# Kernel tuning notes

Measured on AMD Instinct MI355X. Metric: run time of the kernel, lower is better.

The kernel has to match this reference:

```python
import jax, jax.numpy as jnp
import numpy as np

B, S, D = 16, 2048, 128

def setup_inputs() -> dict:
    key = jax.random.key(0)
    kq, kk, kv = jax.random.split(key, 3)
    return {
        "query": jax.random.normal(kq, (B, S, D), dtype=jnp.float32),
        "key": jax.random.normal(kk, (B, S, D), dtype=jnp.float32),
        "value": jax.random.normal(kv, (B, S, D), dtype=jnp.float32),
    }

def reference(query, key, value):
    # query: (B, S2, d), key: (B, S1, d), value: (B, S1, d)
    d_k = query.shape[-1]
    scale = 1.0 / jnp.sqrt(jnp.asarray(d_k, dtype=query.dtype))
    # (B, S2, S1) attention scores
    att = jnp.einsum('bqd,bkd->bqk', query, key) * scale
    att = jax.nn.softmax(att, axis=-1)
    # (B, S2, d_v)
    return jnp.einsum('bqk,bkd->bqd', att, value)
```

## Files before the change

kernel.cpp:

```cpp
#include <hip/hip_runtime.h>

#define B_N 16
#define S_LEN 2048
#define D_DIM 128
#define TK 32
#define NTH 32

typedef __attribute__((ext_vector_type(16))) float f32x16;
typedef __attribute__((ext_vector_type(8)))  short short8;
typedef __attribute__((ext_vector_type(4)))  int   i32x4;
typedef const __attribute__((address_space(1))) void* gp1;
typedef __attribute__((address_space(3))) void* sp3;
#define GLL(g, l) __builtin_amdgcn_global_load_lds((gp1)(const void*)(g), (sp3)(void*)(l), 16, 0, 0)

static __device__ __forceinline__ unsigned short f2bf(float f) {
  unsigned u = __builtin_bit_cast(unsigned, f);
  return (unsigned short)((u + 0x7fffu + ((u >> 16) & 1u)) >> 16);
}

__global__ __launch_bounds__(256)
void prep_kernel(const float* __restrict__ K, const float* __restrict__ V,
                 unsigned short* __restrict__ Kb, unsigned short* __restrict__ VT) {
  __shared__ unsigned short lds[64 * 66];
  int bx = blockIdx.x;
  int t  = threadIdx.x;
  if (bx < 1024) {
#pragma unroll
    for (int rep = 0; rep < 4; ++rep) {
      size_t i = (((size_t)rep * 1024 + bx) * 256 + t) * 4;
      float4 v = *(const float4*)(K + i);
      unsigned lo = (unsigned)f2bf(v.x) | ((unsigned)f2bf(v.y) << 16);
      unsigned hi = (unsigned)f2bf(v.z) | ((unsigned)f2bf(v.w) << 16);
      *(uint2*)(Kb + i) = make_uint2(lo, hi);
    }
  } else {
    int bi = bx - 1024;
    int b  = bi & 15;
    int st = (bi >> 4) & 31;
    int dt = bi >> 9;
    const float* Vb = V + ((size_t)b * S_LEN + st * 64) * D_DIM + dt * 64;
    unsigned short* VTb = VT + ((size_t)b * D_DIM + dt * 64) * S_LEN + st * 64;
#pragma unroll
    for (int rep = 0; rep < 4; ++rep) {
      int idx = rep * 256 + t;
      int i  = idx >> 4;
      int j4 = (idx & 15) * 4;
      float4 v = *(const float4*)(Vb + (size_t)i * D_DIM + j4);
      unsigned lo = (unsigned)f2bf(v.x) | ((unsigned)f2bf(v.y) << 16);
      unsigned hi = (unsigned)f2bf(v.z) | ((unsigned)f2bf(v.w) << 16);
      *(uint2*)&lds[i * 66 + j4] = make_uint2(lo, hi);
    }
    __syncthreads();
#pragma unroll
    for (int rep = 0; rep < 4; ++rep) {
      int idx = rep * 256 + t;
      int dd = idx >> 4;
      int s4 = (idx & 15) * 4;
      unsigned short e0 = lds[(s4 + 0) * 66 + dd];
      unsigned short e1 = lds[(s4 + 1) * 66 + dd];
      unsigned short e2 = lds[(s4 + 2) * 66 + dd];
      unsigned short e3 = lds[(s4 + 3) * 66 + dd];
      *(uint2*)(VTb + (size_t)dd * S_LEN + s4) =
          make_uint2((unsigned)e0 | ((unsigned)e1 << 16),
                     (unsigned)e2 | ((unsigned)e3 << 16));
    }
  }
}

__global__ __launch_bounds__(512, 2)
void attn_kernel(const float* __restrict__ Q, const unsigned short* __restrict__ Kb,
                 const unsigned short* __restrict__ VT, float* __restrict__ O) {
  __shared__ __align__(16) char smem[131072];

  const int tid  = threadIdx.x;
  const int wave = tid >> 6;
  const int g    = wave >> 2;
  const int w4   = wave & 3;
  const int lane = tid & 63;
  const int l32  = lane & 31;
  const int half = lane >> 5;

  const int i     = blockIdx.x;
  const int b     = (i & 7) * 2 + ((i >> 3) & 1);
  const int qtile = i >> 4;
  const int qbase = qtile * 128 + w4 * 32;

  const float* Qb = Q + (size_t)b * S_LEN * D_DIM;
  const unsigned short* Kbb = Kb + (size_t)b * S_LEN * D_DIM;
  const unsigned short* VTb = VT + (size_t)b * D_DIM * S_LEN;

  unsigned short* kb0 = (unsigned short*)smem + (size_t)g * 4 * 4096;
  unsigned short* vb0 = (unsigned short*)(smem + 65536) + (size_t)g * 4 * 4096;

#define ISSUE_TILE(tt, buf)                                                        \
  {                                                                                \
    const int T_ = g * NTH + (tt);                                                 \
    _Pragma("unroll")                                                              \
    for (int cc = 0; cc < 2; ++cc) {                                               \
      int c = w4 * 2 + cc;                                                         \
      int rl = 4 * c + (lane >> 4);                                                \
      int lbk = (lane & 15) ^ (rl & 15);                                           \
      GLL(Kbb + (size_t)(T_ * TK + rl) * D_DIM + lbk * 8, kb0 + (buf) * 4096 + c * 512); \
      int dv = 16 * c + (lane >> 2);                                               \
      int lbv = (lane & 3) ^ ((dv >> 1) & 3);                                      \
      GLL(VTb + (size_t)dv * S_LEN + T_ * TK + lbv * 8, vb0 + (buf) * 4096 + c * 512);   \
    }                                                                              \
  }

#define QK_TILE(buf, saccv)                                                        \
  {                                                                                \
    const unsigned short* kbc_ = kb0 + (buf) * 4096;                               \
    __builtin_amdgcn_s_setprio(1);                                                 \
    _Pragma("unroll")                                                              \
    for (int ks = 0; ks < 8; ++ks) {                                               \
      int pk = (ks * 2 + half) ^ (l32 & 15);                                       \
      short8 kf = *(const short8*)&kbc_[l32 * D_DIM + pk * 8];                     \
      saccv = __builtin_amdgcn_mfma_f32_32x32x16_bf16(kf, qa[ks], saccv, 0, 0, 0); \
    }                                                                              \
    __builtin_amdgcn_s_setprio(0);                                                 \
  }

#define SOFTMAX(saccv, pf0v, pf1v)                                                 \
  {                                                                                \
    float p_[16];                                                                  \
    _Pragma("unroll")                                                              \
    for (int reg = 0; reg < 16; ++reg) {                                           \
      p_[reg] = exp2f(saccv[reg] * SC);                                            \
      lsum += p_[reg];                                                             \
    }                                                                              \
    int dw_[8];                                                                    \
    _Pragma("unroll")                                                              \
    for (int i2 = 0; i2 < 8; ++i2)                                                 \
      asm("v_cvt_pk_bf16_f32 %0, %1, %2"                                           \
          : "=v"(dw_[i2]) : "v"(p_[2 * i2]), "v"(p_[2 * i2 + 1]));                 \
    asm("v_permlane32_swap_b32 %0, %1" : "+v"(dw_[0]), "+v"(dw_[2]));              \
    asm("v_permlane32_swap_b32 %0, %1" : "+v"(dw_[1]), "+v"(dw_[3]));              \
    asm("v_permlane32_swap_b32 %0, %1" : "+v"(dw_[4]), "+v"(dw_[6]));              \
    asm("v_permlane32_swap_b32 %0, %1" : "+v"(dw_[5]), "+v"(dw_[7]));              \
    i32x4 f0_ = {dw_[0], dw_[1], dw_[2], dw_[3]};                                  \
    i32x4 f1_ = {dw_[4], dw_[5], dw_[6], dw_[7]};                                  \
    pf0v = __builtin_bit_cast(short8, f0_);                                        \
    pf1v = __builtin_bit_cast(short8, f1_);                                        \
  }

#define PV_TILE(buf, pf0v, pf1v)                                                   \
  {                                                                                \
    const unsigned short* vbc_ = vb0 + (buf) * 4096;                               \
    __builtin_amdgcn_s_setprio(1);                                                 \
    _Pragma("unroll")                                                              \
    for (int dt = 0; dt < 4; ++dt) {                                               \
      int dv = dt * 32 + l32;                                                      \
      int pv0 = half ^ ((dv >> 1) & 3);                                            \
      short8 vf0 = *(const short8*)&vbc_[dv * TK + pv0 * 8];                       \
      oacc[dt] = __builtin_amdgcn_mfma_f32_32x32x16_bf16(pf0v, vf0, oacc[dt], 0, 0, 0); \
      int pv1 = (2 + half) ^ ((dv >> 1) & 3);                                      \
      short8 vf1 = *(const short8*)&vbc_[dv * TK + pv1 * 8];                       \
      oacc[dt] = __builtin_amdgcn_mfma_f32_32x32x16_bf16(pf1v, vf1, oacc[dt], 0, 0, 0); \
    }                                                                              \
    __builtin_amdgcn_s_setprio(0);                                                 \
  }

  short8 qa[8];
  {
    const float* qp = Qb + (size_t)(qbase + l32) * D_DIM + half * 8;
#pragma unroll
    for (int ks = 0; ks < 8; ++ks) {
      float4 a0 = *(const float4*)(qp + ks * 16);
      float4 a1 = *(const float4*)(qp + ks * 16 + 4);
      short8 f;
      f[0] = (short)f2bf(a0.x); f[1] = (short)f2bf(a0.y);
      f[2] = (short)f2bf(a0.z); f[3] = (short)f2bf(a0.w);
      f[4] = (short)f2bf(a1.x); f[5] = (short)f2bf(a1.y);
      f[6] = (short)f2bf(a1.z); f[7] = (short)f2bf(a1.w);
      qa[ks] = f;
    }
  }

  ISSUE_TILE(0, 0)
  ISSUE_TILE(1, 1)
  ISSUE_TILE(2, 2)

  const f32x16 zf16 = {0.f,0.f,0.f,0.f,0.f,0.f,0.f,0.f,0.f,0.f,0.f,0.f,0.f,0.f,0.f,0.f};
  f32x16 oacc[4];
  float lsum = 0.f;
#pragma unroll
  for (int dt = 0; dt < 4; ++dt) oacc[dt] = zf16;

  const float SC = 0.08838834764831845f * 1.4426950408889634f;

  f32x16 saccA = zf16, saccB;
  short8 pfA0, pfA1, pfB0, pfB1;

  asm volatile("s_waitcnt vmcnt(8)" ::: "memory");
  __builtin_amdgcn_s_barrier();
  QK_TILE(0, saccA)

  for (int t = 0; t + 3 < NTH; t += 2) {
    SOFTMAX(saccA, pfA0, pfA1)
    asm volatile("s_waitcnt vmcnt(4)" ::: "memory");
    __builtin_amdgcn_s_barrier();
    ISSUE_TILE(t + 3, (t + 3) & 3)
    saccB = zf16;
    QK_TILE((t + 1) & 3, saccB)
    PV_TILE(t & 3, pfA0, pfA1)

    SOFTMAX(saccB, pfB0, pfB1)
    asm volatile("s_waitcnt vmcnt(4)" ::: "memory");
    __builtin_amdgcn_s_barrier();
    if (t + 4 < NTH) ISSUE_TILE(t + 4, (t + 4) & 3)
    saccA = zf16;
    QK_TILE((t + 2) & 3, saccA)
    PV_TILE((t + 1) & 3, pfB0, pfB1)
  }

  SOFTMAX(saccA, pfA0, pfA1)
  asm volatile("s_waitcnt vmcnt(0)" ::: "memory");
  __builtin_amdgcn_s_barrier();
  saccB = zf16;
  QK_TILE(31 & 3, saccB)
  PV_TILE(30 & 3, pfA0, pfA1)
  SOFTMAX(saccB, pfB0, pfB1)
  PV_TILE(31 & 3, pfB0, pfB1)

#undef ISSUE_TILE
#undef QK_TILE
#undef SOFTMAX
#undef PV_TILE

  lsum += __shfl_xor(lsum, 32);

  __syncthreads();
  float* mo  = (float*)(smem + w4 * 16640);
  float* ml1 = (float*)(smem + w4 * 16640 + 16384);
  float* ml0 = ml1 + 32;
  if (g == 1) {
#pragma unroll
    for (int reg = 0; reg < 16; ++reg) {
      int row = (reg & 3) + 8 * (reg >> 2) + 4 * half;
#pragma unroll
      for (int dt = 0; dt < 4; ++dt)
        mo[row * 128 + dt * 32 + l32] = oacc[dt][reg];
    }
    if (half == 0) ml1[l32] = lsum;
  } else {
    if (half == 0) ml0[l32] = lsum;
  }
  __syncthreads();
  if (g == 0) {
    float* Ob = O + (size_t)b * S_LEN * D_DIM;
#pragma unroll
    for (int reg = 0; reg < 16; ++reg) {
      int row = (reg & 3) + 8 * (reg >> 2) + 4 * half;
      float linv = 1.f / (ml0[row] + ml1[row]);
#pragma unroll
      for (int dt = 0; dt < 4; ++dt)
        Ob[(size_t)(qbase + row) * D_DIM + dt * 32 + l32] =
            (oacc[dt][reg] + mo[row * 128 + dt * 32 + l32]) * linv;
    }
  }
}

extern "C" void kernel_launch(void* const* d_in, const int* in_sizes, int n_in,
                              void* d_out, int out_size, void* d_ws, size_t ws_size,
                              hipStream_t stream) {
  const float* Q = (const float*)d_in[0];
  const float* K = (const float*)d_in[1];
  const float* V = (const float*)d_in[2];
  float* O = (float*)d_out;
  unsigned short* Kb = (unsigned short*)d_ws;
  unsigned short* VT = Kb + (size_t)B_N * S_LEN * D_DIM;
  prep_kernel<<<dim3(1024 + 1024), dim3(256), 0, stream>>>(K, V, Kb, VT);
  attn_kernel<<<dim3(256), dim3(512), 0, stream>>>(Q, Kb, VT, O);
}
```

Before: 138.6 us.

## Replace 4-deep 32-key tile pipeline with double-buffered 64-key phases

```diff
diff --git a/kernel.cpp b/kernel.cpp
--- a/kernel.cpp
+++ b/kernel.cpp
@@ -4,7 +4,7 @@
 #define S_LEN 2048
 #define D_DIM 128
 #define TK 32
-#define NTH 32
+#define NPH 16
 
 typedef __attribute__((ext_vector_type(16))) float f32x16;
 typedef __attribute__((ext_vector_type(8)))  short short8;
@@ -89,35 +89,45 @@
   const unsigned short* Kbb = Kb + (size_t)b * S_LEN * D_DIM;
   const unsigned short* VTb = VT + (size_t)b * D_DIM * S_LEN;
 
-  unsigned short* kb0 = (unsigned short*)smem + (size_t)g * 4 * 4096;
-  unsigned short* vb0 = (unsigned short*)(smem + 65536) + (size_t)g * 4 * 4096;
-
-#define ISSUE_TILE(tt, buf)                                                        \
-  {                                                                                \
-    const int T_ = g * NTH + (tt);                                                 \
-    _Pragma("unroll")                                                              \
-    for (int cc = 0; cc < 2; ++cc) {                                               \
-      int c = w4 * 2 + cc;                                                         \
-      int rl = 4 * c + (lane >> 4);                                                \
-      int lbk = (lane & 15) ^ (rl & 15);                                           \
-      GLL(Kbb + (size_t)(T_ * TK + rl) * D_DIM + lbk * 8, kb0 + (buf) * 4096 + c * 512); \
-      int dv = 16 * c + (lane >> 2);                                               \
-      int lbv = (lane & 3) ^ ((dv >> 1) & 3);                                      \
-      GLL(VTb + (size_t)dv * S_LEN + T_ * TK + lbv * 8, vb0 + (buf) * 4096 + c * 512);   \
-    }                                                                              \
-  }
-
-#define QK_TILE(buf, saccv)                                                        \
-  {                                                                                \
-    const unsigned short* kbc_ = kb0 + (buf) * 4096;                               \
-    __builtin_amdgcn_s_setprio(1);                                                 \
+  unsigned short* kb0 = (unsigned short*)smem + (size_t)g * 16384;
+  unsigned short* vb0 = (unsigned short*)(smem + 65536) + (size_t)g * 16384;
+
+#define ISSUE_PH(pp, buf)                                                          \
+  {                                                                                \
+    const int kb_ = g * 1024 + (pp) * 64;                                          \
+    _Pragma("unroll")                                                              \
+    for (int ss = 0; ss < 2; ++ss) {                                               \
+      _Pragma("unroll")                                                            \
+      for (int cc = 0; cc < 2; ++cc) {                                             \
+        int c = w4 * 2 + cc;                                                       \
+        int rl = 4 * c + (lane >> 4);                                              \
+        int lbk = (lane & 15) ^ (rl & 15);                                         \
+        GLL(Kbb + (size_t)(kb_ + ss * 32 + rl) * D_DIM + lbk * 8,                  \
+            kb0 + (buf) * 8192 + ss * 4096 + c * 512);                             \
+      }                                                                            \
+    }                                                                              \
+    _Pragma("unroll")                                                              \
+    for (int ss = 0; ss < 2; ++ss) {                                               \
+      _Pragma("unroll")                                                            \
+      for (int cc = 0; cc < 2; ++cc) {                                             \
+        int c = w4 * 2 + cc;                                                       \
+        int dv = 16 * c + (lane >> 2);                                             \
+        int lbv = (lane & 3) ^ ((dv >> 1) & 3);                                    \
+        GLL(VTb + (size_t)dv * S_LEN + kb_ + ss * 32 + lbv * 8,                    \
+            vb0 + (buf) * 8192 + ss * 4096 + c * 512);                             \
+      }                                                                            \
+    }                                                                              \
+  }
+
+#define QK_SUB(buf, ss, saccv)                                                     \
+  {                                                                                \
+    const unsigned short* kbc_ = kb0 + (buf) * 8192 + (ss) * 4096;                 \
     _Pragma("unroll")                                                              \
     for (int ks = 0; ks < 8; ++ks) {                                               \
       int pk = (ks * 2 + half) ^ (l32 & 15);                                       \
       short8 kf = *(const short8*)&kbc_[l32 * D_DIM + pk * 8];                     \
       saccv = __builtin_amdgcn_mfma_f32_32x32x16_bf16(kf, qa[ks], saccv, 0, 0, 0); \
     }                                                                              \
-    __builtin_amdgcn_s_setprio(0);                                                 \
   }
 
 #define SOFTMAX(saccv, pf0v, pf1v)                                                 \
@@ -143,10 +153,9 @@
     pf1v = __builtin_bit_cast(short8, f1_);                                        \
   }
 
-#define PV_TILE(buf, pf0v, pf1v)                                                   \
-  {                                                                                \
-    const unsigned short* vbc_ = vb0 + (buf) * 4096;                               \
-    __builtin_amdgcn_s_setprio(1);                                                 \
+#define PV_SUB(buf, ss, pf0v, pf1v)                                                \
+  {                                                                                \
+    const unsigned short* vbc_ = vb0 + (buf) * 8192 + (ss) * 4096;                 \
     _Pragma("unroll")                                                              \
     for (int dt = 0; dt < 4; ++dt) {                                               \
       int dv = dt * 32 + l32;                                                      \
@@ -157,7 +166,6 @@
       short8 vf1 = *(const short8*)&vbc_[dv * TK + pv1 * 8];                       \
       oacc[dt] = __builtin_amdgcn_mfma_f32_32x32x16_bf16(pf1v, vf1, oacc[dt], 0, 0, 0); \
     }                                                                              \
-    __builtin_amdgcn_s_setprio(0);                                                 \
   }
 
   short8 qa[8];
@@ -176,9 +184,8 @@
     }
   }
 
-  ISSUE_TILE(0, 0)
-  ISSUE_TILE(1, 1)
-  ISSUE_TILE(2, 2)
+  ISSUE_PH(0, 0)
+  ISSUE_PH(1, 1)
 
   const f32x16 zf16 = {0.f,0.f,0.f,0.f,0.f,0.f,0.f,0.f,0.f,0.f,0.f,0.f,0.f,0.f,0.f,0.f};
   f32x16 oacc[4];
@@ -188,44 +195,33 @@
 
   const float SC = 0.08838834764831845f * 1.4426950408889634f;
 
-  f32x16 saccA = zf16, saccB;
-  short8 pfA0, pfA1, pfB0, pfB1;
-
-  asm volatile("s_waitcnt vmcnt(8)" ::: "memory");
-  __builtin_amdgcn_s_barrier();
-  QK_TILE(0, saccA)
-
-  for (int t = 0; t + 3 < NTH; t += 2) {
-    SOFTMAX(saccA, pfA0, pfA1)
-    asm volatile("s_waitcnt vmcnt(4)" ::: "memory");
+  for (int t = 0; t < NPH; ++t) {
+    if (t + 1 < NPH) {
+      asm volatile("s_waitcnt vmcnt(8)" ::: "memory");
+    } else {
+      asm volatile("s_waitcnt vmcnt(0)" ::: "memory");
+    }
     __builtin_amdgcn_s_barrier();
-    ISSUE_TILE(t + 3, (t + 3) & 3)
-    saccB = zf16;
-    QK_TILE((t + 1) & 3, saccB)
-    PV_TILE(t & 3, pfA0, pfA1)
-
-    SOFTMAX(saccB, pfB0, pfB1)
-    asm volatile("s_waitcnt vmcnt(4)" ::: "memory");
+
+    const int cb = t & 1;
+
+    f32x16 sacc0 = zf16, sacc1 = zf16;
+    short8 pf00, pf01, pf10, pf11;
+
+    QK_SUB(cb, 0, sacc0)
+    QK_SUB(cb, 1, sacc1)
+    SOFTMAX(sacc0, pf00, pf01)
+    PV_SUB(cb, 0, pf00, pf01)
+    SOFTMAX(sacc1, pf10, pf11)
+    PV_SUB(cb, 1, pf10, pf11)
+
     __builtin_amdgcn_s_barrier();
-    if (t + 4 < NTH) ISSUE_TILE(t + 4, (t + 4) & 3)
-    saccA = zf16;
-    QK_TILE((t + 2) & 3, saccA)
-    PV_TILE((t + 1) & 3, pfB0, pfB1)
-  }
-
-  SOFTMAX(saccA, pfA0, pfA1)
-  asm volatile("s_waitcnt vmcnt(0)" ::: "memory");
-  __builtin_amdgcn_s_barrier();
-  saccB = zf16;
-  QK_TILE(31 & 3, saccB)
-  PV_TILE(30 & 3, pfA0, pfA1)
-  SOFTMAX(saccB, pfB0, pfB1)
-  PV_TILE(31 & 3, pfB0, pfB1)
-
-#undef ISSUE_TILE
-#undef QK_TILE
+    if (t + 2 < NPH) ISSUE_PH(t + 2, cb)
+  }
+#undef ISSUE_PH
+#undef QK_SUB
 #undef SOFTMAX
-#undef PV_TILE
+#undef PV_SUB
 
   lsum += __shfl_xor(lsum, 32);
 
```

After: 139.1 us. Within noise of the previous version (+0.4%).
